# Kernel optimization log

Hardware: AMD Instinct MI355X
Metric: run time of the kernel (lower is better)

## Reference

```python
import jax, jax.numpy as jnp
import numpy as np

HIDDEN = 1024
HEADS = 16
HEAD_DIM = HIDDEN // HEADS
B, S = 2, 2048


def setup_inputs() -> dict:
    key = jax.random.key(0)
    k1, k2, k3 = jax.random.split(key, 3)
    x = jax.random.normal(k1, (B, S, HIDDEN), dtype=jnp.float32)
    qkv_w = jax.random.normal(k2, (3 * HIDDEN, HIDDEN), dtype=jnp.float32) * (HIDDEN ** -0.5)
    out_w = jax.random.normal(k3, (HIDDEN, HIDDEN), dtype=jnp.float32) * (HIDDEN ** -0.5)
    return {"x": x, "qkv_w": qkv_w, "out_w": out_w}


def reference(x, qkv_w, out_w):
    b, s, d = x.shape
    scale = HEAD_DIM ** -0.5
    # qkv projection (Linear without bias: x @ W^T)
    qkv = x @ qkv_w.T                                   # [b, s, 3d]
    qkv = qkv.reshape(b, s, 3, HEADS, HEAD_DIM)
    qkv = jnp.transpose(qkv, (2, 0, 3, 1, 4))           # [3, b, h, s, hd]
    q, k, v = qkv[0] * scale, qkv[1], qkv[2]
    # causal attention (blocked torch loop == full causal softmax attention)
    scores = jnp.einsum('bhqd,bhkd->bhqk', q, k)        # [b, h, s, s]
    causal = jnp.tril(jnp.ones((s, s), dtype=bool))
    scores = jnp.where(causal[None, None], scores, -jnp.inf)
    weights = jax.nn.softmax(scores, axis=-1)
    attn = jnp.einsum('bhqk,bhkd->bhqd', weights, v)    # [b, h, s, hd]
    attn = jnp.transpose(attn, (0, 2, 1, 3)).reshape(b, s, d)
    return attn @ out_w.T
```

## Files before the change

kernel.cpp:

```cpp
#include <hip/hip_runtime.h>
#include <hip/hip_bf16.h>
#include <math.h>

#define HIDDEN 1024
#define HEADS 16
#define HDIM 64
#define BATCH 2
#define SEQ 2048
#define BHN (BATCH*HEADS)
#define MTOT (BATCH*SEQ)

typedef __attribute__((ext_vector_type(8))) short short8;
typedef __attribute__((ext_vector_type(4))) short short4v;
typedef __attribute__((ext_vector_type(4))) float floatx4;

#define GL2LDS(gsrc, ldst) __builtin_amdgcn_global_load_lds( \
    (const __attribute__((address_space(1))) void*)(gsrc), \
    (__attribute__((address_space(3))) void*)(ldst), 16, 0, 0)

__device__ __forceinline__ short f2bf(float f) {
  union { float f; unsigned u; } v; v.f = f;
  unsigned u = v.u;
  unsigned r = (u + 0x7fffu + ((u >> 16) & 1u)) >> 16;
  return (short)r;
}

__global__ __launch_bounds__(256) void cvt3_f32_bf16(
    const float* __restrict__ a, const float* __restrict__ b, const float* __restrict__ c,
    short* __restrict__ oa, short* __restrict__ ob, short* __restrict__ oc) {
  int i = blockIdx.x * 256 + threadIdx.x;
  const float* src; short* dst; int j;
  if (i < 1048576)      { src = a; dst = oa; j = i; }
  else if (i < 1835008) { src = b; dst = ob; j = i - 1048576; }
  else                  { src = c; dst = oc; j = i - 1835008; }
  float4 f = reinterpret_cast<const float4*>(src)[j];
  short4 o;
  o.x = f2bf(f.x); o.y = f2bf(f.y); o.z = f2bf(f.z); o.w = f2bf(f.w);
  reinterpret_cast<short4*>(dst)[j] = o;
}

template<int EPI, int BN>
__global__ __launch_bounds__(256) void gemm_bt(
    const short* __restrict__ A, const short* __restrict__ B,
    int M, int N, int K,
    float* __restrict__ outF,
    short* __restrict__ outQ, short* __restrict__ outK, short* __restrict__ outV)
{
  constexpr int WN = BN / 2;
  constexpr int NI = BN / 32;
  __shared__ __align__(16) short As[128*64];
  __shared__ __align__(16) short Bs[BN*64];
  const int tid = threadIdx.x;
  const int wv = tid >> 6;
  const int lane = tid & 63;
  const int l15 = lane & 15;
  const int quad = lane >> 4;
  const int swl = l15 & 7;
  const int wm = wv >> 1, wn = wv & 1;
  const int row0 = blockIdx.y * 128, col0 = blockIdx.x * BN;

  floatx4 acc[4][NI];
#pragma unroll
  for (int i = 0; i < 4; i++)
#pragma unroll
    for (int j = 0; j < NI; j++) acc[i][j] = (floatx4){0.f, 0.f, 0.f, 0.f};

  for (int k0 = 0; k0 < K; k0 += 64) {
#pragma unroll
    for (int rd = 0; rd < 4; ++rd) {
      int chunk = rd * 256 + tid;
      int r = chunk >> 3, c = ((chunk & 7) ^ (r & 7)) << 3;
      GL2LDS(A + (long)(row0 + r) * K + k0 + c, As + (rd * 256 + wv * 64) * 8);
    }
#pragma unroll
    for (int rd = 0; rd < BN / 32; ++rd) {
      int chunk = rd * 256 + tid;
      int r = chunk >> 3, c = ((chunk & 7) ^ (r & 7)) << 3;
      GL2LDS(B + (long)(col0 + r) * K + k0 + c, Bs + (rd * 256 + wv * 64) * 8);
    }
    __syncthreads();

    short8 af[4][2], bfr[NI][2];
#pragma unroll
    for (int mi = 0; mi < 4; mi++) {
      const short* ap = As + (wm * 64 + mi * 16 + l15) * 64;
#pragma unroll
      for (int kk = 0; kk < 2; kk++)
        af[mi][kk] = *(const short8*)(ap + (((kk * 4 + quad) ^ swl) << 3));
    }
#pragma unroll
    for (int ni = 0; ni < NI; ni++) {
      const short* bp = Bs + (wn * WN + ni * 16 + l15) * 64;
#pragma unroll
      for (int kk = 0; kk < 2; kk++)
        bfr[ni][kk] = *(const short8*)(bp + (((kk * 4 + quad) ^ swl) << 3));
    }
#pragma unroll
    for (int mi = 0; mi < 4; mi++)
#pragma unroll
      for (int ni = 0; ni < NI; ni++)
#pragma unroll
        for (int kk = 0; kk < 2; kk++)
          acc[mi][ni] = __builtin_amdgcn_mfma_f32_16x16x32_bf16(af[mi][kk], bfr[ni][kk], acc[mi][ni], 0, 0, 0);
    __syncthreads();
  }

  if (EPI == 2) {
#pragma unroll
    for (int mi = 0; mi < 4; mi++) {
      int rr = row0 + wm * 64 + mi * 16 + quad * 4;
#pragma unroll
      for (int ni = 0; ni < NI; ni++) {
        int cc = col0 + wn * WN + ni * 16 + l15;
#pragma unroll
        for (int r = 0; r < 4; r++)
          outF[(long)(rr + r) * N + cc] = acc[mi][ni][r];
      }
    }
  } else {
#pragma unroll
    for (int mi = 0; mi < 4; mi++) {
      int rowg = row0 + wm * 64 + mi * 16 + quad * 4;
#pragma unroll
      for (int ni = 0; ni < NI; ni++) {
        int j = col0 + wn * WN + ni * 16 + l15;
        int t = j >> 10;
        int rem = j & 1023;
        int h = rem >> 6, d = rem & 63;
#pragma unroll
        for (int r = 0; r < 4; r++) {
          int i = rowg + r;
          int b = i >> 11, s = i & 2047;
          int bh = b * HEADS + h;
          float v = acc[mi][ni][r];
          if (t == 0)      outQ[(bh * SEQ + s) * HDIM + d] = f2bf(v * 0.18033688011112042f);
          else if (t == 1) outK[(bh * SEQ + s) * HDIM + d] = f2bf(v);
          else             outV[(bh * HDIM + d) * SEQ + s] = f2bf(v);
        }
      }
    }
  }
}

__device__ __forceinline__ void stage_kv(const short* __restrict__ kg,
                                         const short* __restrict__ vT,
                                         int bh, int kt, short* KsB, short* VsB,
                                         int tid, int wv) {
#pragma unroll
  for (int i = 0; i < 2; ++i) {
    int slot = i * 256 + tid;
    int r = slot >> 3;
    int c = ((slot & 7) ^ (r & 7)) << 3;
    GL2LDS(kg + (bh * SEQ + kt * 64 + r) * HDIM + c, KsB + (i * 256 + wv * 64) * 8);
    GL2LDS(vT + (bh * HDIM + r) * SEQ + kt * 64 + c, VsB + (i * 256 + wv * 64) * 8);
  }
}

__global__ __launch_bounds__(256, 4) void flash_attn(
    const short* __restrict__ qg, const short* __restrict__ kg,
    const short* __restrict__ vT, short* __restrict__ attn)
{
  __shared__ __align__(16) short Ks[2][64 * 64];
  __shared__ __align__(16) short Vs[2][64 * 64];

  const int tid = threadIdx.x;
  const int wv = tid >> 6, lane = tid & 63;
  const int l15 = lane & 15, quad = lane >> 4;
  const int bh = blockIdx.x;
  const int yl = (int)blockIdx.y;
  const int sgrp = yl >> 3, y0 = yl & 7;
  const int yp = ((sgrp >> 1) << 4) + ((sgrp & 1) ? (15 - y0) : y0);
  const int rt = 31 - yp;
  const int qh = wv >> 1;
  const int kh = wv & 1;
  const int m0 = rt * 64 + qh * 32;
  const int swl = l15 & 7;

  short8 aq[2][2];
#pragma unroll
  for (int g = 0; g < 2; g++) {
    const short* qp = qg + (long)(bh * SEQ + m0 + g * 16 + l15) * HDIM + quad * 8;
    aq[g][0] = *(const short8*)qp;
    aq[g][1] = *(const short8*)(qp + 32);
  }

  const short ONE = (short)0x3F80;
  const short4v ones4 = {ONE, ONE, ONE, ONE};

  floatx4 o[2][4], lsum[2];
#pragma unroll
  for (int g = 0; g < 2; g++) {
    lsum[g] = (floatx4){0.f, 0.f, 0.f, 0.f};
#pragma unroll
    for (int nt = 0; nt < 4; nt++) o[g][nt] = (floatx4){0.f, 0.f, 0.f, 0.f};
  }

  const int ntiles = rt + 1;
  stage_kv(kg, vT, bh, 0, Ks[0], Vs[0], tid, wv);

  for (int kt = 0; kt < ntiles; ++kt) {
    __syncthreads();
    const int buf = kt & 1;
    if (kt + 1 < ntiles)
      stage_kv(kg, vT, bh, kt + 1, Ks[buf ^ 1], Vs[buf ^ 1], tid, wv);

    const short* KsB = Ks[buf];
    const short* VsB = Vs[buf];

    floatx4 sc[2][2];
#pragma unroll
    for (int g = 0; g < 2; g++)
#pragma unroll
      for (int sub = 0; sub < 2; sub++) sc[g][sub] = (floatx4){0.f, 0.f, 0.f, 0.f};
    __builtin_amdgcn_s_setprio(1);
#pragma unroll
    for (int sub = 0; sub < 2; sub++) {
      const short* kp = KsB + (kh * 32 + sub * 16 + l15) * 64;
      short8 kf0 = *(const short8*)(kp + ((quad ^ swl) << 3));
      short8 kf1 = *(const short8*)(kp + (((4 + quad) ^ swl) << 3));
#pragma unroll
      for (int g = 0; g < 2; g++) {
        sc[g][sub] = __builtin_amdgcn_mfma_f32_16x16x32_bf16(kf0, aq[g][0], sc[g][sub], 0, 0, 0);
        sc[g][sub] = __builtin_amdgcn_mfma_f32_16x16x32_bf16(kf1, aq[g][1], sc[g][sub], 0, 0, 0);
      }
    }
    __builtin_amdgcn_s_setprio(0);

    short4v pa[2][2];
#pragma unroll
    for (int g = 0; g < 2; g++) {
      const int qrow = m0 + g * 16 + l15;
#pragma unroll
      for (int sub = 0; sub < 2; sub++) {
        const int kbase = kt * 64 + kh * 32 + sub * 16;
        const bool full = (kbase + 15) <= (m0 + g * 16);
        unsigned u[4];
#pragma unroll
        for (int r = 0; r < 4; r++) {
          float pe = __builtin_amdgcn_exp2f(sc[g][sub][r]);
          if (!full) {
            const int kpos = kbase + quad * 4 + r;
            pe = (kpos <= qrow) ? pe : 0.f;
          }
          u[r] = __builtin_bit_cast(unsigned, pe) & 0xffff0000u;
        }
        uint2 w;
        w.x = (u[0] >> 16) | u[1];
        w.y = (u[2] >> 16) | u[3];
        pa[g][sub] = __builtin_bit_cast(short4v, w);
      }
    }

    __builtin_amdgcn_s_setprio(1);
#pragma unroll
    for (int sub = 0; sub < 2; sub++) {
      short4v bv[4];
#pragma unroll
      for (int nt = 0; nt < 4; nt++) {
        const int ch = (kh * 4 + sub * 2 + (quad >> 1)) ^ swl;
        bv[nt] = *(const short4v*)(VsB + (nt * 16 + l15) * 64 + (ch << 3) + ((quad & 1) << 2));
      }
#pragma unroll
      for (int g = 0; g < 2; g++) {
        lsum[g] = __builtin_amdgcn_mfma_f32_16x16x16bf16_1k(pa[g][sub], ones4, lsum[g], 0, 0, 0);
#pragma unroll
        for (int nt = 0; nt < 4; nt++)
          o[g][nt] = __builtin_amdgcn_mfma_f32_16x16x16bf16_1k(pa[g][sub], bv[nt], o[g][nt], 0, 0, 0);
      }
    }
    __builtin_amdgcn_s_setprio(0);
  }

  __syncthreads();
  float* redO = (float*)&Ks[0][0];
  float* redL = (float*)&Vs[0][0];
  if (kh == 1) {
#pragma unroll
    for (int g = 0; g < 2; g++) {
      const int base = (qh * 64 + lane) * 2 + g;
#pragma unroll
      for (int nt = 0; nt < 4; nt++)
#pragma unroll
        for (int r = 0; r < 4; r++)
          redO[base * 16 + nt * 4 + r] = o[g][nt][r];
#pragma unroll
      for (int r = 0; r < 4; r++) redL[base * 4 + r] = lsum[g][r];
    }
  }
  __syncthreads();
  if (kh == 0) {
    const int b = bh >> 4, h = bh & 15;
#pragma unroll
    for (int g = 0; g < 2; g++) {
      const int base = (qh * 64 + lane) * 2 + g;
      floatx4 lt = lsum[g];
#pragma unroll
      for (int r = 0; r < 4; r++) lt[r] += redL[base * 4 + r];
#pragma unroll
      for (int r = 0; r < 4; r++) {
        const float inv = 1.0f / lt[r];
        const int srow = m0 + g * 16 + quad * 4 + r;
#pragma unroll
        for (int nt = 0; nt < 4; nt++) {
          float val = o[g][nt][r] + redO[base * 16 + nt * 4 + r];
          attn[(long)(b * SEQ + srow) * HIDDEN + h * HDIM + nt * 16 + l15] = f2bf(val * inv);
        }
      }
    }
  }
}

extern "C" void kernel_launch(void* const* d_in, const int* in_sizes, int n_in,
                              void* d_out, int out_size, void* d_ws, size_t ws_size,
                              hipStream_t stream) {
  const float* x     = (const float*)d_in[0];
  const float* qkv_w = (const float*)d_in[1];
  const float* out_w = (const float*)d_in[2];
  float* out = (float*)d_out;

  short* xb   = (short*)d_ws;
  short* wqb  = xb  + MTOT * HIDDEN;
  short* wob  = wqb + 3 * HIDDEN * HIDDEN;
  short* qB   = wob + HIDDEN * HIDDEN;
  short* kB   = qB  + BHN * SEQ * HDIM;
  short* vTB  = kB  + BHN * SEQ * HDIM;
  short* attn = vTB + BHN * SEQ * HDIM;

  cvt3_f32_bf16<<<dim3(8192), dim3(256), 0, stream>>>(x, qkv_w, out_w, xb, wqb, wob);

  gemm_bt<1, 128><<<dim3(3 * HIDDEN / 128, MTOT / 128), dim3(256), 0, stream>>>(
      xb, wqb, MTOT, 3 * HIDDEN, HIDDEN, nullptr, qB, kB, vTB);

  flash_attn<<<dim3(BHN, SEQ / 64), dim3(256), 0, stream>>>(qB, kB, vTB, attn);

  gemm_bt<2, 64><<<dim3(HIDDEN / 64, MTOT / 128), dim3(256), 0, stream>>>(
      attn, wob, MTOT, HIDDEN, HIDDEN, out, nullptr, nullptr, nullptr);
}
```

Baseline: 173.6 us.

## Double-buffer GEMM LDS tiles with K=32 steps and prefetch next stage

The bf16 GEMM now uses two LDS buffers with a K-step of 32 instead of one buffer with a K-step of 64. It issues the global-to-LDS load for the next step before computing the current one, with a single barrier per iteration. This is meant to overlap global memory latency with MFMA work, and it raises wave priority around the MFMA block. In exchange there are twice as many loop iterations and barriers, with fewer MFMAs per sync, and the XOR swizzle changes to 4-chunk rows, which could raise LDS bank conflicts.

```diff
diff --git a/kernel.cpp b/kernel.cpp
--- a/kernel.cpp
+++ b/kernel.cpp
@@ -48,14 +48,15 @@
 {
   constexpr int WN = BN / 2;
   constexpr int NI = BN / 32;
-  __shared__ __align__(16) short As[128*64];
-  __shared__ __align__(16) short Bs[BN*64];
+  constexpr int ARD = 2;
+  constexpr int BRD = BN / 64;
+  __shared__ __align__(16) short As[2][128 * 32];
+  __shared__ __align__(16) short Bs[2][BN * 32];
   const int tid = threadIdx.x;
   const int wv = tid >> 6;
   const int lane = tid & 63;
   const int l15 = lane & 15;
   const int quad = lane >> 4;
-  const int swl = l15 & 7;
   const int wm = wv >> 1, wn = wv & 1;
   const int row0 = blockIdx.y * 128, col0 = blockIdx.x * BN;
 
@@ -65,45 +66,53 @@
 #pragma unroll
     for (int j = 0; j < NI; j++) acc[i][j] = (floatx4){0.f, 0.f, 0.f, 0.f};
 
-  for (int k0 = 0; k0 < K; k0 += 64) {
-#pragma unroll
-    for (int rd = 0; rd < 4; ++rd) {
-      int chunk = rd * 256 + tid;
-      int r = chunk >> 3, c = ((chunk & 7) ^ (r & 7)) << 3;
-      GL2LDS(A + (long)(row0 + r) * K + k0 + c, As + (rd * 256 + wv * 64) * 8);
-    }
-#pragma unroll
-    for (int rd = 0; rd < BN / 32; ++rd) {
-      int chunk = rd * 256 + tid;
-      int r = chunk >> 3, c = ((chunk & 7) ^ (r & 7)) << 3;
-      GL2LDS(B + (long)(col0 + r) * K + k0 + c, Bs + (rd * 256 + wv * 64) * 8);
-    }
+  const int nsteps = K >> 5;
+
+#define STAGE_GEMM(t, bsel)                                                         \
+  do {                                                                              \
+    int k0 = (t) << 5;                                                              \
+    _Pragma("unroll")                                                               \
+    for (int rd = 0; rd < ARD; ++rd) {                                              \
+      int chunk = rd * 256 + tid;                                                   \
+      int r = chunk >> 2, c = ((chunk & 3) ^ (r & 3)) << 3;                         \
+      GL2LDS(A + (long)(row0 + r) * K + k0 + c, &As[bsel][(rd * 256 + wv * 64) * 8]); \
+    }                                                                               \
+    _Pragma("unroll")                                                               \
+    for (int rd = 0; rd < BRD; ++rd) {                                              \
+      int chunk = rd * 256 + tid;                                                   \
+      int r = chunk >> 2, c = ((chunk & 3) ^ (r & 3)) << 3;                         \
+      GL2LDS(B + (long)(col0 + r) * K + k0 + c, &Bs[bsel][(rd * 256 + wv * 64) * 8]); \
+    }                                                                               \
+  } while (0)
+
+  STAGE_GEMM(0, 0);
+
+  for (int t = 0; t < nsteps; ++t) {
+    const int buf = t & 1;
     __syncthreads();
-
-    short8 af[4][2], bfr[NI][2];
+    if (t + 1 < nsteps)
+      STAGE_GEMM(t + 1, buf ^ 1);
+
+    short8 af[4], bfr[NI];
 #pragma unroll
     for (int mi = 0; mi < 4; mi++) {
-      const short* ap = As + (wm * 64 + mi * 16 + l15) * 64;
-#pragma unroll
-      for (int kk = 0; kk < 2; kk++)
-        af[mi][kk] = *(const short8*)(ap + (((kk * 4 + quad) ^ swl) << 3));
+      const int r = wm * 64 + mi * 16 + l15;
+      af[mi] = *(const short8*)(&As[buf][r * 32 + ((quad ^ (r & 3)) << 3)]);
     }
 #pragma unroll
     for (int ni = 0; ni < NI; ni++) {
-      const short* bp = Bs + (wn * WN + ni * 16 + l15) * 64;
-#pragma unroll
-      for (int kk = 0; kk < 2; kk++)
-        bfr[ni][kk] = *(const short8*)(bp + (((kk * 4 + quad) ^ swl) << 3));
-    }
+      const int r = wn * WN + ni * 16 + l15;
+      bfr[ni] = *(const short8*)(&Bs[buf][r * 32 + ((quad ^ (r & 3)) << 3)]);
+    }
+    __builtin_amdgcn_s_setprio(1);
 #pragma unroll
     for (int mi = 0; mi < 4; mi++)
 #pragma unroll
       for (int ni = 0; ni < NI; ni++)
-#pragma unroll
-        for (int kk = 0; kk < 2; kk++)
-          acc[mi][ni] = __builtin_amdgcn_mfma_f32_16x16x32_bf16(af[mi][kk], bfr[ni][kk], acc[mi][ni], 0, 0, 0);
-    __syncthreads();
-  }
+        acc[mi][ni] = __builtin_amdgcn_mfma_f32_16x16x32_bf16(af[mi], bfr[ni], acc[mi][ni], 0, 0, 0);
+    __builtin_amdgcn_s_setprio(0);
+  }
+#undef STAGE_GEMM
 
   if (EPI == 2) {
 #pragma unroll
```

Result: slower. 177.4 us (+2.2%).

## Split-K the output projection with atomic adds and precompute GEMM load pointers

Applied to the files above, without the earlier changes.

The output projection GEMM is now split along K into two partitions on a third grid dimension, and partial results are combined with atomic float adds. The output buffer is zeroed inside the conversion kernel. The GEMM also precomputes per-thread global source pointers outside the K loop and raises wave priority around the MFMA block. The aim is to double the block count for the small output GEMM (512 to 1024 blocks) so the GPU is better filled, at the cost of extra atomic traffic and non-deterministic summation order.

```diff
diff --git a/kernel.cpp b/kernel.cpp
--- a/kernel.cpp
+++ b/kernel.cpp
@@ -27,10 +27,11 @@
 
 __global__ __launch_bounds__(256) void cvt3_f32_bf16(
     const float* __restrict__ a, const float* __restrict__ b, const float* __restrict__ c,
-    short* __restrict__ oa, short* __restrict__ ob, short* __restrict__ oc) {
+    short* __restrict__ oa, short* __restrict__ ob, short* __restrict__ oc,
+    float4* __restrict__ oz) {
   int i = blockIdx.x * 256 + threadIdx.x;
   const float* src; short* dst; int j;
-  if (i < 1048576)      { src = a; dst = oa; j = i; }
+  if (i < 1048576)      { src = a; dst = oa; j = i; oz[j] = (float4){0.f, 0.f, 0.f, 0.f}; }
   else if (i < 1835008) { src = b; dst = ob; j = i - 1048576; }
   else                  { src = c; dst = oc; j = i - 1835008; }
   float4 f = reinterpret_cast<const float4*>(src)[j];
@@ -39,7 +40,7 @@
   reinterpret_cast<short4*>(dst)[j] = o;
 }
 
-template<int EPI, int BN>
+template<int EPI, int BN, int SPLITK>
 __global__ __launch_bounds__(256) void gemm_bt(
     const short* __restrict__ A, const short* __restrict__ B,
     int M, int N, int K,
@@ -48,6 +49,7 @@
 {
   constexpr int WN = BN / 2;
   constexpr int NI = BN / 32;
+  constexpr int BRD = BN / 32;
   __shared__ __align__(16) short As[128*64];
   __shared__ __align__(16) short Bs[BN*64];
   const int tid = threadIdx.x;
@@ -58,6 +60,24 @@
   const int swl = l15 & 7;
   const int wm = wv >> 1, wn = wv & 1;
   const int row0 = blockIdx.y * 128, col0 = blockIdx.x * BN;
+  const int Kpart = K / SPLITK;
+  const int kBase = (SPLITK > 1) ? (int)blockIdx.z * Kpart : 0;
+  const int nsteps = Kpart >> 6;
+
+  const short* aSrc[4];
+#pragma unroll
+  for (int rd = 0; rd < 4; ++rd) {
+    int chunk = rd * 256 + tid;
+    int r = chunk >> 3, c = ((chunk & 7) ^ (r & 7)) << 3;
+    aSrc[rd] = A + (long)(row0 + r) * K + kBase + c;
+  }
+  const short* bSrc[BRD];
+#pragma unroll
+  for (int rd = 0; rd < BRD; ++rd) {
+    int chunk = rd * 256 + tid;
+    int r = chunk >> 3, c = ((chunk & 7) ^ (r & 7)) << 3;
+    bSrc[rd] = B + (long)(col0 + r) * K + kBase + c;
+  }
 
   floatx4 acc[4][NI];
 #pragma unroll
@@ -65,18 +85,16 @@
 #pragma unroll
     for (int j = 0; j < NI; j++) acc[i][j] = (floatx4){0.f, 0.f, 0.f, 0.f};
 
-  for (int k0 = 0; k0 < K; k0 += 64) {
+  for (int t = 0; t < nsteps; ++t) {
 #pragma unroll
     for (int rd = 0; rd < 4; ++rd) {
-      int chunk = rd * 256 + tid;
-      int r = chunk >> 3, c = ((chunk & 7) ^ (r & 7)) << 3;
-      GL2LDS(A + (long)(row0 + r) * K + k0 + c, As + (rd * 256 + wv * 64) * 8);
-    }
-#pragma unroll
-    for (int rd = 0; rd < BN / 32; ++rd) {
-      int chunk = rd * 256 + tid;
-      int r = chunk >> 3, c = ((chunk & 7) ^ (r & 7)) << 3;
-      GL2LDS(B + (long)(col0 + r) * K + k0 + c, Bs + (rd * 256 + wv * 64) * 8);
+      GL2LDS(aSrc[rd], As + (rd * 256 + wv * 64) * 8);
+      aSrc[rd] += 64;
+    }
+#pragma unroll
+    for (int rd = 0; rd < BRD; ++rd) {
+      GL2LDS(bSrc[rd], Bs + (rd * 256 + wv * 64) * 8);
+      bSrc[rd] += 64;
     }
     __syncthreads();
 
@@ -95,6 +113,7 @@
       for (int kk = 0; kk < 2; kk++)
         bfr[ni][kk] = *(const short8*)(bp + (((kk * 4 + quad) ^ swl) << 3));
     }
+    __builtin_amdgcn_s_setprio(1);
 #pragma unroll
     for (int mi = 0; mi < 4; mi++)
 #pragma unroll
@@ -102,10 +121,11 @@
 #pragma unroll
         for (int kk = 0; kk < 2; kk++)
           acc[mi][ni] = __builtin_amdgcn_mfma_f32_16x16x32_bf16(af[mi][kk], bfr[ni][kk], acc[mi][ni], 0, 0, 0);
+    __builtin_amdgcn_s_setprio(0);
     __syncthreads();
   }
 
-  if (EPI == 2) {
+  if (EPI == 2 || EPI == 3) {
 #pragma unroll
     for (int mi = 0; mi < 4; mi++) {
       int rr = row0 + wm * 64 + mi * 16 + quad * 4;
@@ -113,8 +133,10 @@
       for (int ni = 0; ni < NI; ni++) {
         int cc = col0 + wn * WN + ni * 16 + l15;
 #pragma unroll
-        for (int r = 0; r < 4; r++)
-          outF[(long)(rr + r) * N + cc] = acc[mi][ni][r];
+        for (int r = 0; r < 4; r++) {
+          if (EPI == 2) outF[(long)(rr + r) * N + cc] = acc[mi][ni][r];
+          else          unsafeAtomicAdd(&outF[(long)(rr + r) * N + cc], acc[mi][ni][r]);
+        }
       }
     }
   } else {
@@ -326,13 +348,14 @@
   short* vTB  = kB  + BHN * SEQ * HDIM;
   short* attn = vTB + BHN * SEQ * HDIM;
 
-  cvt3_f32_bf16<<<dim3(8192), dim3(256), 0, stream>>>(x, qkv_w, out_w, xb, wqb, wob);
-
-  gemm_bt<1, 128><<<dim3(3 * HIDDEN / 128, MTOT / 128), dim3(256), 0, stream>>>(
+  cvt3_f32_bf16<<<dim3(8192), dim3(256), 0, stream>>>(x, qkv_w, out_w, xb, wqb, wob,
+                                                      (float4*)out);
+
+  gemm_bt<1, 128, 1><<<dim3(3 * HIDDEN / 128, MTOT / 128), dim3(256), 0, stream>>>(
       xb, wqb, MTOT, 3 * HIDDEN, HIDDEN, nullptr, qB, kB, vTB);
 
   flash_attn<<<dim3(BHN, SEQ / 64), dim3(256), 0, stream>>>(qB, kB, vTB, attn);
 
-  gemm_bt<2, 64><<<dim3(HIDDEN / 64, MTOT / 128), dim3(256), 0, stream>>>(
+  gemm_bt<3, 64, 2><<<dim3(HIDDEN / 64, MTOT / 128, 2), dim3(256), 0, stream>>>(
       attn, wob, MTOT, HIDDEN, HIDDEN, out, nullptr, nullptr, nullptr);
 }
```

Measured after the change: 189.2 us. 9.0% more time.
